# Kernel tuning notes

Hardware: AMD Instinct MI355X
Metric: run time of the kernel (lower is better)

Reference implementation:

```python
import jax, jax.numpy as jnp
import numpy as np

NUM_HEADS = 8
HEAD_SIZE = 64  # hidden_dim // num_heads = 512 // 8
SCALE = 1.0 / np.sqrt(HEAD_SIZE).astype(np.float32)
CAUSAL = True


def setup_inputs() -> dict:
    key = jax.random.key(0)
    k1, k2, k3 = jax.random.split(key, 3)
    b, s, d = 4, 2048, 512
    x = jax.random.normal(k1, (b, s, d), dtype=jnp.float32)
    w_qkv = jax.random.normal(k2, (d, 3 * d), dtype=jnp.float32) * 0.02
    b_qkv = jnp.zeros((3 * d,), dtype=jnp.float32)
    w_out = jax.random.normal(k3, (d, d), dtype=jnp.float32) * 0.02
    b_out = jnp.zeros((d,), dtype=jnp.float32)
    return {"x": x, "w_qkv": w_qkv, "b_qkv": b_qkv, "w_out": w_out, "b_out": b_out}


def reference(x, w_qkv, b_qkv, w_out, b_out):
    b, s, d = x.shape
    h, hd = NUM_HEADS, HEAD_SIZE
    qkv = x @ w_qkv + b_qkv                      # (b, s, 3d)
    q, k, v = jnp.split(qkv, 3, axis=-1)
    # (b, s, d) -> (b, h, s, hd)
    q = q.reshape(b, s, h, hd).transpose(0, 2, 1, 3)
    k = k.reshape(b, s, h, hd).transpose(0, 2, 1, 3)
    v = v.reshape(b, s, h, hd).transpose(0, 2, 1, 3)
    scores = jnp.einsum('bhqd,bhkd->bhqk', q, k) * SCALE  # (b, h, s, s)
    if CAUSAL:
        causal_mask = jnp.triu(jnp.ones((s, s), dtype=bool), k=1)
        scores = jnp.where(causal_mask, -jnp.inf, scores)
    attn = jax.nn.softmax(scores, axis=-1)
    out = jnp.einsum('bhqk,bhkd->bhqd', attn, v)          # (b, h, s, hd)
    out = out.transpose(0, 2, 1, 3).reshape(b, s, d)
    return out @ w_out + b_out
```

## Files before the change

### kernel.cpp

```cpp
#include <hip/hip_runtime.h>

#define BATCH 4
#define SEQ   2048
#define DM    512
#define NH    8
#define HD    64
#define PART  (BATCH*NH*SEQ*HD)
#define QSCALE 0.18033688f

typedef unsigned short u16;
typedef unsigned int   u32;
typedef __bf16 bf16x8 __attribute__((ext_vector_type(8)));
typedef float  f32x4  __attribute__((ext_vector_type(4)));

__device__ __forceinline__ u16 f2bf(float f) {
    union { float f; u32 u; } v; v.f = f;
    u32 r = v.u + 0x7fffu + ((v.u >> 16) & 1u);
    return (u16)(r >> 16);
}

__device__ __forceinline__ void glds16(const u16* g, u16* lds) {
    __builtin_amdgcn_global_load_lds(
        (const __attribute__((address_space(1))) void*)g,
        (__attribute__((address_space(3))) void*)lds, 16, 0, 0);
}

__global__ __launch_bounds__(256) void prep_k(
    const float* __restrict__ x, u16* __restrict__ xb,
    const float* __restrict__ w_qkv, u16* __restrict__ t_qkv,
    const float* __restrict__ w_out, u16* __restrict__ t_out)
{
    __shared__ u16 Ts[64][72];
    const int z = blockIdx.z, bx = blockIdx.x, t = threadIdx.x;

    if (z == 0) {
        const int n8 = PART / 8;
        for (int i = bx * 256 + t; i < n8; i += 512 * 256) {
            float4 a = *(const float4*)(x + (size_t)i * 8);
            float4 b = *(const float4*)(x + (size_t)i * 8 + 4);
            union { uint4 v; u16 s[8]; } o;
            o.s[0] = f2bf(a.x); o.s[1] = f2bf(a.y);
            o.s[2] = f2bf(a.z); o.s[3] = f2bf(a.w);
            o.s[4] = f2bf(b.x); o.s[5] = f2bf(b.y);
            o.s[6] = f2bf(b.z); o.s[7] = f2bf(b.w);
            *(uint4*)(xb + (size_t)i * 8) = o.v;
        }
        return;
    }
    const int N = (z == 1) ? 3 * DM : DM;
    const int ntiles = N / 64;
    if (bx >= ntiles * 8) return;
    const float* W = (z == 1) ? w_qkv : w_out;
    u16* Wt = (z == 1) ? t_qkv : t_out;
    const int n0 = (bx % ntiles) * 64, k0 = (bx / ntiles) * 64;

    #pragma unroll
    for (int l = 0; l < 4; ++l) {
        int idx = l * 1024 + t * 4;
        int r = idx >> 6, c = idx & 63;
        float4 v = *(const float4*)(W + (size_t)(k0 + r) * N + n0 + c);
        Ts[c + 0][r] = f2bf(v.x);
        Ts[c + 1][r] = f2bf(v.y);
        Ts[c + 2][r] = f2bf(v.z);
        Ts[c + 3][r] = f2bf(v.w);
    }
    __syncthreads();
    #pragma unroll
    for (int l = 0; l < 2; ++l) {
        int idx = l * 256 + t;
        int row = idx >> 3, ch = idx & 7;
        *(uint4*)(Wt + (size_t)(n0 + row) * DM + k0 + ch * 8) =
            *(const uint4*)(&Ts[row][ch * 8]);
    }
}

template<int MODE>
__global__ __launch_bounds__(256) void gemm_k(
    const u16* __restrict__ A, const u16* __restrict__ Bt,
    const float* __restrict__ bias, void* __restrict__ outv,
    int M, int N, int K)
{
    __shared__ __align__(16) u16 As[2][128 * 32];
    __shared__ __align__(16) u16 Bs[2][128 * 32];

    const int tid  = threadIdx.x;
    const int bm0  = blockIdx.x * 128;
    const int bn0  = blockIdx.y * 128;
    const int wave = tid >> 6, lane = tid & 63;
    const int l16  = lane & 15, quad = lane >> 4;
    const int wr   = (wave & 1) * 64;
    const int wc   = (wave >> 1) * 64;

    const int srow = (lane >> 2);
    const int scol = (lane & 3) * 8;
    const u16* Ag = A + (size_t)(bm0 + wave * 32 + srow) * K + scol;
    const u16* Bg = Bt + (size_t)(bn0 + wave * 32 + srow) * K + scol;
    const int wofs = (wave * 32) * 32;

    f32x4 acc[4][4];
    #pragma unroll
    for (int i = 0; i < 4; ++i)
        #pragma unroll
        for (int j = 0; j < 4; ++j)
            acc[i][j] = (f32x4){0.f, 0.f, 0.f, 0.f};

    glds16(Ag,                  &As[0][wofs]);
    glds16(Ag + (size_t)16 * K, &As[0][wofs + 16 * 32]);
    glds16(Bg,                  &Bs[0][wofs]);
    glds16(Bg + (size_t)16 * K, &Bs[0][wofs + 16 * 32]);
    __syncthreads();

    const int NIT = K >> 5;
    for (int it = 0; it < NIT; ++it) {
        const int cur = it & 1;
        if (it + 1 < NIT) {
            const int nx = cur ^ 1;
            const int k0 = (it + 1) << 5;
            glds16(Ag + k0,                  &As[nx][wofs]);
            glds16(Ag + k0 + (size_t)16 * K, &As[nx][wofs + 16 * 32]);
            glds16(Bg + k0,                  &Bs[nx][wofs]);
            glds16(Bg + k0 + (size_t)16 * K, &Bs[nx][wofs + 16 * 32]);
        }

        bf16x8 af[4], bfr[4];
        #pragma unroll
        for (int mi = 0; mi < 4; ++mi)
            af[mi] = *(const bf16x8*)(&As[cur][(wr + mi * 16 + l16) * 32 + quad * 8]);
        #pragma unroll
        for (int ni = 0; ni < 4; ++ni)
            bfr[ni] = *(const bf16x8*)(&Bs[cur][(wc + ni * 16 + l16) * 32 + quad * 8]);
        #pragma unroll
        for (int mi = 0; mi < 4; ++mi)
            #pragma unroll
            for (int ni = 0; ni < 4; ++ni)
                acc[mi][ni] = __builtin_amdgcn_mfma_f32_16x16x32_bf16(
                    af[mi], bfr[ni], acc[mi][ni], 0, 0, 0);
        __syncthreads();
    }

    #pragma unroll
    for (int mi = 0; mi < 4; ++mi) {
        #pragma unroll
        for (int ni = 0; ni < 4; ++ni) {
            int col = bn0 + wc + ni * 16 + l16;
            float bv = bias[col];
            int row0 = bm0 + wr + mi * 16 + quad * 4;
            float v[4];
            #pragma unroll
            for (int reg = 0; reg < 4; ++reg) v[reg] = acc[mi][ni][reg] + bv;

            if (MODE == 1) {
                #pragma unroll
                for (int reg = 0; reg < 4; ++reg)
                    ((float*)outv)[(size_t)(row0 + reg) * N + col] = v[reg];
            } else {
                u16* ws = (u16*)outv;
                int part = col >> 9, wi = col & 511;
                int h = wi >> 6, e = wi & 63;
                int b = row0 >> 11, s0 = row0 & 2047;
                if (part == 2) {
                    union { u16 q[4]; uint2 u; } pk;
                    #pragma unroll
                    for (int reg = 0; reg < 4; ++reg) pk.q[reg] = f2bf(v[reg]);
                    *(uint2*)(ws + (size_t)2 * PART +
                              ((size_t)(b * NH + h) * HD + e) * SEQ + s0) = pk.u;
                } else {
                    float scl = (part == 0) ? QSCALE : 1.0f;
                    #pragma unroll
                    for (int reg = 0; reg < 4; ++reg)
                        ws[(size_t)part * PART +
                           ((size_t)(b * NH + h) * SEQ + s0 + reg) * HD + e] =
                            f2bf(v[reg] * scl);
                }
            }
        }
    }
}

__global__ __launch_bounds__(256) void attn_k(
    const u16* __restrict__ Q, const u16* __restrict__ K,
    const u16* __restrict__ Vt, u16* __restrict__ O)
{
    __shared__ __align__(16) u16 KsB[2][64 * 64];
    __shared__ __align__(16) u16 VtB[2][64 * 64];
    __shared__ __align__(16) u16 Ps[128][72];

    const int bh = blockIdx.x;
    const int yy = blockIdx.y;
    const int qb = (yy < 8) ? (15 - yy) : (yy - 8);
    const int tid = threadIdx.x, wave = tid >> 6, lane = tid & 63;
    const int l16 = lane & 15, quad = lane >> 4;
    const size_t baseK = (size_t)bh * SEQ * HD;
    const size_t baseV = (size_t)bh * HD * SEQ;
    const size_t baseQ = baseK + (size_t)qb * 128 * HD;

    #pragma unroll
    for (int r = 0; r < 4; ++r) {
        int chunk = r * 256 + tid;
        int row = chunk >> 3, c8 = (chunk & 7) << 3;
        *(uint4*)(&Ps[row][c8]) = *(const uint4*)(Q + baseQ + row * 64 + c8);
    }
    __syncthreads();

    bf16x8 qf[2][2];
    #pragma unroll
    for (int rf = 0; rf < 2; ++rf)
        #pragma unroll
        for (int d0 = 0; d0 < 2; ++d0)
            qf[rf][d0] = *(const bf16x8*)(&Ps[rf * 64 + wave * 16 + l16]
                                            [d0 * 32 + quad * 8]);

    const int sub = lane >> 3;
    const int lcx = (lane & 7) ^ sub;
    const u16* kg = K  + baseK + (size_t)((wave * 16 + sub) * 64)   + lcx * 8;
    const u16* vg = Vt + baseV + (size_t)((wave * 16 + sub) * 2048) + lcx * 8;
    u16* ksd = &KsB[0][wave * 1024];
    u16* vtd = &VtB[0][wave * 1024];

    glds16(kg,            ksd);
    glds16(kg + 8 * 64,   ksd + 512);
    glds16(vg,            vtd);
    glds16(vg + 8 * 2048, vtd + 512);
    __syncthreads();

    float l_part[2][4];
    f32x4 o_acc[2][4];
    #pragma unroll
    for (int rf = 0; rf < 2; ++rf)
        #pragma unroll
        for (int i = 0; i < 4; ++i) {
            l_part[rf][i] = 0.f;
            o_acc[rf][i] = (f32x4){0.f, 0.f, 0.f, 0.f};
        }

    const int last = 2 * qb + 1;
    const int row64 = wave * 16 + quad * 4;

    for (int kt = 0; kt <= last; ++kt) {
        const int cur = kt & 1;

        if (kt < last) {
            const int nx = (cur ^ 1) * 4096;
            glds16(kg + (size_t)(kt + 1) * 4096,          ksd + nx);
            glds16(kg + (size_t)(kt + 1) * 4096 + 8 * 64, ksd + nx + 512);
            glds16(vg + (size_t)(kt + 1) * 64,            vtd + nx);
            glds16(vg + (size_t)(kt + 1) * 64 + 8 * 2048, vtd + nx + 512);
        }

        bf16x8 kf[2][4], vf[2][4];
        #pragma unroll
        for (int d0 = 0; d0 < 2; ++d0)
            #pragma unroll
            for (int nt = 0; nt < 4; ++nt) {
                int pc = (d0 * 4 + quad) ^ (l16 & 7);
                kf[d0][nt] = *(const bf16x8*)
                    (&KsB[cur][(nt * 16 + l16) * 64 + pc * 8]);
                vf[d0][nt] = *(const bf16x8*)
                    (&VtB[cur][(nt * 16 + l16) * 64 + pc * 8]);
            }

        #pragma unroll
        for (int rf = 0; rf < 2; ++rf) {
            if (kt == last && rf == 0) continue;
            f32x4 s[4];
            #pragma unroll
            for (int nt = 0; nt < 4; ++nt) s[nt] = (f32x4){0.f, 0.f, 0.f, 0.f};
            #pragma unroll
            for (int d0 = 0; d0 < 2; ++d0)
                #pragma unroll
                for (int nt = 0; nt < 4; ++nt)
                    s[nt] = __builtin_amdgcn_mfma_f32_16x16x32_bf16(
                        qf[rf][d0], kf[d0][nt], s[nt], 0, 0, 0);

            const bool diag = (kt == 2 * qb + rf);
            #pragma unroll
            for (int nt = 0; nt < 4; ++nt) {
                int cl = nt * 16 + l16;
                #pragma unroll
                for (int reg = 0; reg < 4; ++reg) {
                    float p = __builtin_amdgcn_exp2f(s[nt][reg]);
                    if (diag && cl > row64 + reg) p = 0.f;
                    l_part[rf][reg] += p;
                    Ps[rf * 64 + row64 + reg][cl] = f2bf(p);
                }
            }

            #pragma unroll
            for (int k0 = 0; k0 < 2; ++k0) {
                bf16x8 ap = *(const bf16x8*)
                    (&Ps[rf * 64 + wave * 16 + l16][k0 * 32 + quad * 8]);
                #pragma unroll
                for (int dt = 0; dt < 4; ++dt)
                    o_acc[rf][dt] = __builtin_amdgcn_mfma_f32_16x16x32_bf16(
                        ap, vf[k0][dt], o_acc[rf][dt], 0, 0, 0);
            }
        }
        __syncthreads();
    }

    const int b = bh >> 3, h = bh & 7;
    #pragma unroll
    for (int rf = 0; rf < 2; ++rf) {
        float l_i[4];
        #pragma unroll
        for (int reg = 0; reg < 4; ++reg) {
            float l = l_part[rf][reg];
            #pragma unroll
            for (int off = 1; off < 16; off <<= 1)
                l += __shfl_xor(l, off);
            l_i[reg] = l;
        }
        #pragma unroll
        for (int dt = 0; dt < 4; ++dt) {
            #pragma unroll
            for (int reg = 0; reg < 4; ++reg) {
                int srow = qb * 128 + rf * 64 + row64 + reg;
                float v = o_acc[rf][dt][reg] / l_i[reg];
                size_t idx = (((size_t)(b * SEQ + srow)) * NH + h) * HD
                             + dt * 16 + l16;
                O[idx] = f2bf(v);
            }
        }
    }
}

extern "C" void kernel_launch(void* const* d_in, const int* in_sizes, int n_in,
                              void* d_out, int out_size, void* d_ws, size_t ws_size,
                              hipStream_t stream) {
    const float* x     = (const float*)d_in[0];
    const float* w_qkv = (const float*)d_in[1];
    const float* b_qkv = (const float*)d_in[2];
    const float* w_out = (const float*)d_in[3];
    const float* b_out = (const float*)d_in[4];

    u16* qkv    = (u16*)d_ws;
    u16* attn   = qkv + (size_t)3 * PART;
    u16* xb     = attn + (size_t)PART;
    u16* wt_qkv = xb + (size_t)PART;
    u16* wt_out = wt_qkv + (size_t)(3 * DM) * DM;

    const int M = BATCH * SEQ;

    prep_k<<<dim3(512, 1, 3), 256, 0, stream>>>(x, xb, w_qkv, wt_qkv,
                                                w_out, wt_out);

    dim3 g1(M / 128, (3 * DM) / 128);
    gemm_k<0><<<g1, 256, 0, stream>>>(xb, wt_qkv, b_qkv, qkv, M, 3 * DM, DM);

    dim3 g2(BATCH * NH, 16);
    attn_k<<<g2, 256, 0, stream>>>(qkv, qkv + PART, qkv + 2 * (size_t)PART, attn);

    dim3 g3(M / 128, DM / 128);
    gemm_k<1><<<g3, 256, 0, stream>>>(attn, wt_out, b_out, (float*)d_out, M, DM, DM);
}
```

Measured before the change: 166.8 us.

## Load K/V fragments directly from global into registers, drop LDS staging

Replaces the LDS double-buffered K/Vt staging (global_load_lds) with direct per-lane global loads into register fragments. K is prefetched one tile ahead in registers and V is loaded at the top of each iteration. This removes the per-iteration __syncthreads and shrinks LDS, and the kernel also asks for 2 blocks per CU in launch bounds. It also packs bf16 conversion with the hardware pair conversion. The cost is redundant global/L2 traffic, since every wave reloads the full K/V tiles, plus exposed V load latency and extra register pressure.

After: 250.7 us. 1.5x slower.

```diff
diff --git a/kernel.cpp b/kernel.cpp
--- a/kernel.cpp
+++ b/kernel.cpp
@@ -1,4 +1,5 @@
 #include <hip/hip_runtime.h>
+#include <hip/hip_bf16.h>
 
 #define BATCH 4
 #define SEQ   2048
@@ -177,12 +178,10 @@
     }
 }
 
-__global__ __launch_bounds__(256) void attn_k(
+__global__ __launch_bounds__(256, 2) void attn_k(
     const u16* __restrict__ Q, const u16* __restrict__ K,
     const u16* __restrict__ Vt, u16* __restrict__ O)
 {
-    __shared__ __align__(16) u16 KsB[2][64 * 64];
-    __shared__ __align__(16) u16 VtB[2][64 * 64];
     __shared__ __align__(16) u16 Ps[128][72];
 
     const int bh = blockIdx.x;
@@ -209,19 +208,18 @@
         for (int d0 = 0; d0 < 2; ++d0)
             qf[rf][d0] = *(const bf16x8*)(&Ps[rf * 64 + wave * 16 + l16]
                                             [d0 * 32 + quad * 8]);
-
-    const int sub = lane >> 3;
-    const int lcx = (lane & 7) ^ sub;
-    const u16* kg = K  + baseK + (size_t)((wave * 16 + sub) * 64)   + lcx * 8;
-    const u16* vg = Vt + baseV + (size_t)((wave * 16 + sub) * 2048) + lcx * 8;
-    u16* ksd = &KsB[0][wave * 1024];
-    u16* vtd = &VtB[0][wave * 1024];
-
-    glds16(kg,            ksd);
-    glds16(kg + 8 * 64,   ksd + 512);
-    glds16(vg,            vtd);
-    glds16(vg + 8 * 2048, vtd + 512);
     __syncthreads();
+
+    const u16* Kb = K + baseK;
+    const u16* Vb = Vt + baseV;
+
+    bf16x8 kf[2][2][4];
+    #pragma unroll
+    for (int d0 = 0; d0 < 2; ++d0)
+        #pragma unroll
+        for (int nt = 0; nt < 4; ++nt)
+            kf[0][d0][nt] = *(const bf16x8*)
+                (Kb + (size_t)(nt * 16 + l16) * 64 + d0 * 32 + quad * 8);
 
     float l_part[2][4];
     f32x4 o_acc[2][4];
@@ -239,25 +237,24 @@
     for (int kt = 0; kt <= last; ++kt) {
         const int cur = kt & 1;
 
+        bf16x8 vf[2][4];
+        #pragma unroll
+        for (int k0 = 0; k0 < 2; ++k0)
+            #pragma unroll
+            for (int dt = 0; dt < 4; ++dt)
+                vf[k0][dt] = *(const bf16x8*)
+                    (Vb + (size_t)(dt * 16 + l16) * SEQ +
+                     kt * 64 + k0 * 32 + quad * 8);
+
         if (kt < last) {
-            const int nx = (cur ^ 1) * 4096;
-            glds16(kg + (size_t)(kt + 1) * 4096,          ksd + nx);
-            glds16(kg + (size_t)(kt + 1) * 4096 + 8 * 64, ksd + nx + 512);
-            glds16(vg + (size_t)(kt + 1) * 64,            vtd + nx);
-            glds16(vg + (size_t)(kt + 1) * 64 + 8 * 2048, vtd + nx + 512);
-        }
-
-        bf16x8 kf[2][4], vf[2][4];
-        #pragma unroll
-        for (int d0 = 0; d0 < 2; ++d0)
-            #pragma unroll
-            for (int nt = 0; nt < 4; ++nt) {
-                int pc = (d0 * 4 + quad) ^ (l16 & 7);
-                kf[d0][nt] = *(const bf16x8*)
-                    (&KsB[cur][(nt * 16 + l16) * 64 + pc * 8]);
-                vf[d0][nt] = *(const bf16x8*)
-                    (&VtB[cur][(nt * 16 + l16) * 64 + pc * 8]);
-            }
+            #pragma unroll
+            for (int d0 = 0; d0 < 2; ++d0)
+                #pragma unroll
+                for (int nt = 0; nt < 4; ++nt)
+                    kf[cur ^ 1][d0][nt] = *(const bf16x8*)
+                        (Kb + (size_t)((kt + 1) * 64 + nt * 16 + l16) * 64 +
+                         d0 * 32 + quad * 8);
+        }
 
         #pragma unroll
         for (int rf = 0; rf < 2; ++rf) {
@@ -270,19 +267,26 @@
                 #pragma unroll
                 for (int nt = 0; nt < 4; ++nt)
                     s[nt] = __builtin_amdgcn_mfma_f32_16x16x32_bf16(
-                        qf[rf][d0], kf[d0][nt], s[nt], 0, 0, 0);
+                        qf[rf][d0], kf[cur][d0][nt], s[nt], 0, 0, 0);
 
             const bool diag = (kt == 2 * qb + rf);
             #pragma unroll
             for (int nt = 0; nt < 4; ++nt) {
                 int cl = nt * 16 + l16;
+                float p[4];
                 #pragma unroll
                 for (int reg = 0; reg < 4; ++reg) {
-                    float p = __builtin_amdgcn_exp2f(s[nt][reg]);
-                    if (diag && cl > row64 + reg) p = 0.f;
-                    l_part[rf][reg] += p;
-                    Ps[rf * 64 + row64 + reg][cl] = f2bf(p);
+                    p[reg] = __builtin_amdgcn_exp2f(s[nt][reg]);
+                    if (diag && cl > row64 + reg) p[reg] = 0.f;
+                    l_part[rf][reg] += p[reg];
                 }
+                union { __hip_bfloat162 h; u16 s2[2]; } pk01, pk23;
+                pk01.h = __float22bfloat162_rn(float2{p[0], p[1]});
+                pk23.h = __float22bfloat162_rn(float2{p[2], p[3]});
+                Ps[rf * 64 + row64 + 0][cl] = pk01.s2[0];
+                Ps[rf * 64 + row64 + 1][cl] = pk01.s2[1];
+                Ps[rf * 64 + row64 + 2][cl] = pk23.s2[0];
+                Ps[rf * 64 + row64 + 3][cl] = pk23.s2[1];
             }
 
             #pragma unroll
@@ -295,7 +299,6 @@
                         ap, vf[k0][dt], o_acc[rf][dt], 0, 0, 0);
             }
         }
-        __syncthreads();
     }
 
     const int b = bh >> 3, h = bh & 7;
```

## Split attention into paired 64-row query tiles and shrink output GEMM tile

Applied to the files above, without the earlier changes.

The attention kernel now processes two 64-row query tiles per block, pairing a long and a short causal tile, instead of one 128-row tile with two register fragments. This cuts registers and LDS per block and aims for better occupancy and balance, at the cost of reloading K/V per tile. The output-projection GEMM uses 64-row tiles to launch twice as many blocks. Probabilities are packed to bf16 with a paired conversion intrinsic.

Result: faster. 151.1 us (-9.4%).

```diff
diff --git a/kernel.cpp b/kernel.cpp
--- a/kernel.cpp
+++ b/kernel.cpp
@@ -1,4 +1,5 @@
 #include <hip/hip_runtime.h>
+#include <hip/hip_bf16.h>
 
 #define BATCH 4
 #define SEQ   2048
@@ -80,34 +81,39 @@
     const float* __restrict__ bias, void* __restrict__ outv,
     int M, int N, int K)
 {
-    __shared__ __align__(16) u16 As[2][128 * 32];
+    constexpr int BM = (MODE == 1) ? 64 : 128;
+    constexpr int NI = (MODE == 1) ? 2 : 4;
+
+    __shared__ __align__(16) u16 As[2][BM * 32];
     __shared__ __align__(16) u16 Bs[2][128 * 32];
 
     const int tid  = threadIdx.x;
-    const int bm0  = blockIdx.x * 128;
+    const int bm0  = blockIdx.x * BM;
     const int bn0  = blockIdx.y * 128;
     const int wave = tid >> 6, lane = tid & 63;
     const int l16  = lane & 15, quad = lane >> 4;
-    const int wr   = (wave & 1) * 64;
-    const int wc   = (wave >> 1) * 64;
+    const int wr   = (MODE == 1) ? 0 : (wave & 1) * 64;
+    const int wc   = (MODE == 1) ? wave * 32 : (wave >> 1) * 64;
 
     const int srow = (lane >> 2);
     const int scol = (lane & 3) * 8;
-    const u16* Ag = A + (size_t)(bm0 + wave * 32 + srow) * K + scol;
+    const int arow = (MODE == 1) ? (wave * 16) : (wave * 32);
+    const u16* Ag = A + (size_t)(bm0 + arow + srow) * K + scol;
     const u16* Bg = Bt + (size_t)(bn0 + wave * 32 + srow) * K + scol;
-    const int wofs = (wave * 32) * 32;
-
-    f32x4 acc[4][4];
+    const int wofsA = arow * 32;
+    const int wofsB = (wave * 32) * 32;
+
+    f32x4 acc[4][NI];
     #pragma unroll
     for (int i = 0; i < 4; ++i)
         #pragma unroll
-        for (int j = 0; j < 4; ++j)
+        for (int j = 0; j < NI; ++j)
             acc[i][j] = (f32x4){0.f, 0.f, 0.f, 0.f};
 
-    glds16(Ag,                  &As[0][wofs]);
-    glds16(Ag + (size_t)16 * K, &As[0][wofs + 16 * 32]);
-    glds16(Bg,                  &Bs[0][wofs]);
-    glds16(Bg + (size_t)16 * K, &Bs[0][wofs + 16 * 32]);
+    glds16(Ag, &As[0][wofsA]);
+    if (MODE == 0) glds16(Ag + (size_t)16 * K, &As[0][wofsA + 16 * 32]);
+    glds16(Bg,                  &Bs[0][wofsB]);
+    glds16(Bg + (size_t)16 * K, &Bs[0][wofsB + 16 * 32]);
     __syncthreads();
 
     const int NIT = K >> 5;
@@ -116,23 +122,23 @@
         if (it + 1 < NIT) {
             const int nx = cur ^ 1;
             const int k0 = (it + 1) << 5;
-            glds16(Ag + k0,                  &As[nx][wofs]);
-            glds16(Ag + k0 + (size_t)16 * K, &As[nx][wofs + 16 * 32]);
-            glds16(Bg + k0,                  &Bs[nx][wofs]);
-            glds16(Bg + k0 + (size_t)16 * K, &Bs[nx][wofs + 16 * 32]);
-        }
-
-        bf16x8 af[4], bfr[4];
+            glds16(Ag + k0, &As[nx][wofsA]);
+            if (MODE == 0) glds16(Ag + k0 + (size_t)16 * K, &As[nx][wofsA + 16 * 32]);
+            glds16(Bg + k0,                  &Bs[nx][wofsB]);
+            glds16(Bg + k0 + (size_t)16 * K, &Bs[nx][wofsB + 16 * 32]);
+        }
+
+        bf16x8 af[4], bfr[NI];
         #pragma unroll
         for (int mi = 0; mi < 4; ++mi)
             af[mi] = *(const bf16x8*)(&As[cur][(wr + mi * 16 + l16) * 32 + quad * 8]);
         #pragma unroll
-        for (int ni = 0; ni < 4; ++ni)
+        for (int ni = 0; ni < NI; ++ni)
             bfr[ni] = *(const bf16x8*)(&Bs[cur][(wc + ni * 16 + l16) * 32 + quad * 8]);
         #pragma unroll
         for (int mi = 0; mi < 4; ++mi)
             #pragma unroll
-            for (int ni = 0; ni < 4; ++ni)
+            for (int ni = 0; ni < NI; ++ni)
                 acc[mi][ni] = __builtin_amdgcn_mfma_f32_16x16x32_bf16(
                     af[mi], bfr[ni], acc[mi][ni], 0, 0, 0);
         __syncthreads();
@@ -141,7 +147,7 @@
     #pragma unroll
     for (int mi = 0; mi < 4; ++mi) {
         #pragma unroll
-        for (int ni = 0; ni < 4; ++ni) {
+        for (int ni = 0; ni < NI; ++ni) {
             int col = bn0 + wc + ni * 16 + l16;
             float bv = bias[col];
             int row0 = bm0 + wr + mi * 16 + quad * 4;
@@ -183,32 +189,16 @@
 {
     __shared__ __align__(16) u16 KsB[2][64 * 64];
     __shared__ __align__(16) u16 VtB[2][64 * 64];
-    __shared__ __align__(16) u16 Ps[128][72];
+    __shared__ __align__(16) u16 Ps[64][72];
 
     const int bh = blockIdx.x;
-    const int yy = blockIdx.y;
-    const int qb = (yy < 8) ? (15 - yy) : (yy - 8);
+    const int pair = blockIdx.y;
     const int tid = threadIdx.x, wave = tid >> 6, lane = tid & 63;
     const int l16 = lane & 15, quad = lane >> 4;
     const size_t baseK = (size_t)bh * SEQ * HD;
     const size_t baseV = (size_t)bh * HD * SEQ;
-    const size_t baseQ = baseK + (size_t)qb * 128 * HD;
-
-    #pragma unroll
-    for (int r = 0; r < 4; ++r) {
-        int chunk = r * 256 + tid;
-        int row = chunk >> 3, c8 = (chunk & 7) << 3;
-        *(uint4*)(&Ps[row][c8]) = *(const uint4*)(Q + baseQ + row * 64 + c8);
-    }
-    __syncthreads();
-
-    bf16x8 qf[2][2];
-    #pragma unroll
-    for (int rf = 0; rf < 2; ++rf)
-        #pragma unroll
-        for (int d0 = 0; d0 < 2; ++d0)
-            qf[rf][d0] = *(const bf16x8*)(&Ps[rf * 64 + wave * 16 + l16]
-                                            [d0 * 32 + quad * 8]);
+    const int b = bh >> 3, h = bh & 7;
+    const int row64 = wave * 16 + quad * 4;
 
     const int sub = lane >> 3;
     const int lcx = (lane & 7) ^ sub;
@@ -217,51 +207,57 @@
     u16* ksd = &KsB[0][wave * 1024];
     u16* vtd = &VtB[0][wave * 1024];
 
-    glds16(kg,            ksd);
-    glds16(kg + 8 * 64,   ksd + 512);
-    glds16(vg,            vtd);
-    glds16(vg + 8 * 2048, vtd + 512);
-    __syncthreads();
-
-    float l_part[2][4];
-    f32x4 o_acc[2][4];
-    #pragma unroll
-    for (int rf = 0; rf < 2; ++rf)
-        #pragma unroll
-        for (int i = 0; i < 4; ++i) {
-            l_part[rf][i] = 0.f;
-            o_acc[rf][i] = (f32x4){0.f, 0.f, 0.f, 0.f};
-        }
-
-    const int last = 2 * qb + 1;
-    const int row64 = wave * 16 + quad * 4;
-
-    for (int kt = 0; kt <= last; ++kt) {
-        const int cur = kt & 1;
-
-        if (kt < last) {
-            const int nx = (cur ^ 1) * 4096;
-            glds16(kg + (size_t)(kt + 1) * 4096,          ksd + nx);
-            glds16(kg + (size_t)(kt + 1) * 4096 + 8 * 64, ksd + nx + 512);
-            glds16(vg + (size_t)(kt + 1) * 64,            vtd + nx);
-            glds16(vg + (size_t)(kt + 1) * 64 + 8 * 2048, vtd + nx + 512);
-        }
-
-        bf16x8 kf[2][4], vf[2][4];
+    #pragma unroll
+    for (int phase = 0; phase < 2; ++phase) {
+        const int qt = phase ? pair : (31 - pair);
+        const size_t baseQ = baseK + (size_t)qt * 64 * HD;
+
+        #pragma unroll
+        for (int r = 0; r < 2; ++r) {
+            int chunk = r * 256 + tid;
+            int row = chunk >> 3, c8 = (chunk & 7) << 3;
+            *(uint4*)(&Ps[row][c8]) = *(const uint4*)(Q + baseQ + row * 64 + c8);
+        }
+        __syncthreads();
+        bf16x8 qf[2];
         #pragma unroll
         for (int d0 = 0; d0 < 2; ++d0)
-            #pragma unroll
-            for (int nt = 0; nt < 4; ++nt) {
-                int pc = (d0 * 4 + quad) ^ (l16 & 7);
-                kf[d0][nt] = *(const bf16x8*)
-                    (&KsB[cur][(nt * 16 + l16) * 64 + pc * 8]);
-                vf[d0][nt] = *(const bf16x8*)
-                    (&VtB[cur][(nt * 16 + l16) * 64 + pc * 8]);
-            }
-
-        #pragma unroll
-        for (int rf = 0; rf < 2; ++rf) {
-            if (kt == last && rf == 0) continue;
+            qf[d0] = *(const bf16x8*)(&Ps[wave * 16 + l16][d0 * 32 + quad * 8]);
+        __syncthreads();
+
+        glds16(kg,            ksd);
+        glds16(kg + 8 * 64,   ksd + 512);
+        glds16(vg,            vtd);
+        glds16(vg + 8 * 2048, vtd + 512);
+        __syncthreads();
+
+        float l_part[4] = {0.f, 0.f, 0.f, 0.f};
+        f32x4 o_acc[4];
+        #pragma unroll
+        for (int i = 0; i < 4; ++i) o_acc[i] = (f32x4){0.f, 0.f, 0.f, 0.f};
+
+        for (int kt = 0; kt <= qt; ++kt) {
+            const int cur = kt & 1;
+            if (kt < qt) {
+                const int nx = (cur ^ 1) * 4096;
+                glds16(kg + (size_t)(kt + 1) * 4096,          ksd + nx);
+                glds16(kg + (size_t)(kt + 1) * 4096 + 8 * 64, ksd + nx + 512);
+                glds16(vg + (size_t)(kt + 1) * 64,            vtd + nx);
+                glds16(vg + (size_t)(kt + 1) * 64 + 8 * 2048, vtd + nx + 512);
+            }
+
+            bf16x8 kf[2][4], vf[2][4];
+            #pragma unroll
+            for (int d0 = 0; d0 < 2; ++d0)
+                #pragma unroll
+                for (int nt = 0; nt < 4; ++nt) {
+                    int pc = (d0 * 4 + quad) ^ (l16 & 7);
+                    kf[d0][nt] = *(const bf16x8*)
+                        (&KsB[cur][(nt * 16 + l16) * 64 + pc * 8]);
+                    vf[d0][nt] = *(const bf16x8*)
+                        (&VtB[cur][(nt * 16 + l16) * 64 + pc * 8]);
+                }
+
             f32x4 s[4];
             #pragma unroll
             for (int nt = 0; nt < 4; ++nt) s[nt] = (f32x4){0.f, 0.f, 0.f, 0.f};
@@ -270,41 +266,44 @@
                 #pragma unroll
                 for (int nt = 0; nt < 4; ++nt)
                     s[nt] = __builtin_amdgcn_mfma_f32_16x16x32_bf16(
-                        qf[rf][d0], kf[d0][nt], s[nt], 0, 0, 0);
-
-            const bool diag = (kt == 2 * qb + rf);
+                        qf[d0], kf[d0][nt], s[nt], 0, 0, 0);
+
+            const bool diag = (kt == qt);
             #pragma unroll
             for (int nt = 0; nt < 4; ++nt) {
                 int cl = nt * 16 + l16;
+                float p[4];
                 #pragma unroll
                 for (int reg = 0; reg < 4; ++reg) {
-                    float p = __builtin_amdgcn_exp2f(s[nt][reg]);
-                    if (diag && cl > row64 + reg) p = 0.f;
-                    l_part[rf][reg] += p;
-                    Ps[rf * 64 + row64 + reg][cl] = f2bf(p);
+                    p[reg] = __builtin_amdgcn_exp2f(s[nt][reg]);
+                    if (diag && cl > row64 + reg) p[reg] = 0.f;
+                    l_part[reg] += p[reg];
                 }
+                union { __hip_bfloat162 hh; u16 s2[2]; } pk01, pk23;
+                pk01.hh = __float22bfloat162_rn(float2{p[0], p[1]});
+                pk23.hh = __float22bfloat162_rn(float2{p[2], p[3]});
+                Ps[row64 + 0][cl] = pk01.s2[0];
+                Ps[row64 + 1][cl] = pk01.s2[1];
+                Ps[row64 + 2][cl] = pk23.s2[0];
+                Ps[row64 + 3][cl] = pk23.s2[1];
             }
 
             #pragma unroll
             for (int k0 = 0; k0 < 2; ++k0) {
                 bf16x8 ap = *(const bf16x8*)
-                    (&Ps[rf * 64 + wave * 16 + l16][k0 * 32 + quad * 8]);
+                    (&Ps[wave * 16 + l16][k0 * 32 + quad * 8]);
                 #pragma unroll
                 for (int dt = 0; dt < 4; ++dt)
-                    o_acc[rf][dt] = __builtin_amdgcn_mfma_f32_16x16x32_bf16(
-                        ap, vf[k0][dt], o_acc[rf][dt], 0, 0, 0);
-            }
-        }
-        __syncthreads();
-    }
-
-    const int b = bh >> 3, h = bh & 7;
-    #pragma unroll
-    for (int rf = 0; rf < 2; ++rf) {
+                    o_acc[dt] = __builtin_amdgcn_mfma_f32_16x16x32_bf16(
+                        ap, vf[k0][dt], o_acc[dt], 0, 0, 0);
+            }
+            __syncthreads();
+        }
+
         float l_i[4];
         #pragma unroll
         for (int reg = 0; reg < 4; ++reg) {
-            float l = l_part[rf][reg];
+            float l = l_part[reg];
             #pragma unroll
             for (int off = 1; off < 16; off <<= 1)
                 l += __shfl_xor(l, off);
@@ -314,8 +313,8 @@
         for (int dt = 0; dt < 4; ++dt) {
             #pragma unroll
             for (int reg = 0; reg < 4; ++reg) {
-                int srow = qb * 128 + rf * 64 + row64 + reg;
-                float v = o_acc[rf][dt][reg] / l_i[reg];
+                int srow = qt * 64 + row64 + reg;
+                float v = o_acc[dt][reg] / l_i[reg];
                 size_t idx = (((size_t)(b * SEQ + srow)) * NH + h) * HD
                              + dt * 16 + l16;
                 O[idx] = f2bf(v);
@@ -350,6 +349,6 @@
     dim3 g2(BATCH * NH, 16);
     attn_k<<<g2, 256, 0, stream>>>(qkv, qkv + PART, qkv + 2 * (size_t)PART, attn);
 
-    dim3 g3(M / 128, DM / 128);
+    dim3 g3(M / 64, DM / 128);
     gemm_k<1><<<g3, 256, 0, stream>>>(attn, wt_out, b_out, (float*)d_out, M, DM, DM);
 }
```
